# Performance work log

Hardware: AMD Instinct MI355X
Metric: run time of the kernel (lower is better)

## Reference

```python
import jax, jax.numpy as jnp
import numpy as np

BOX_SIDE = 50.0  # orthorhombic simulation cell side length


def setup_inputs() -> dict:
    key = jax.random.key(0)
    k1, _ = jax.random.split(key)
    N = 8192
    pos = jax.random.uniform(k1, (N, 3), dtype=jnp.float32) * BOX_SIDE  # cartesian positions in box
    box = jnp.ones((3,), dtype=jnp.float32) * BOX_SIDE                   # box lengths (orthorhombic)
    return {"pos": pos, "box": box, "k": 17}


def reference(pos, box, k):
    """Periodic (minimum-image) k-NN graph: returns (edge_index [2, N*k], knn_dist [N, k])."""
    N = pos.shape[0]
    # Accumulate squared wrapped distances one spatial dim at a time to avoid an (N,N,3) intermediate.
    d2 = jnp.zeros((N, N), dtype=pos.dtype)
    for d in range(pos.shape[1]):  # fixed small loop over 3 spatial dims
        diff = pos[:, None, d] - pos[None, :, d]
        diff = diff - box[d] * jnp.round(diff / box[d])  # minimum-image wrap
        d2 = d2 + diff * diff
    # Exclude self-edges.
    d2 = jnp.where(jnp.eye(N, dtype=bool), jnp.inf, d2)
    # k nearest neighbors per node (smallest distance => top_k of negated d2).
    _, idx = jax.lax.top_k(-d2, k)                      # idx: [N, k]
    knn_d2 = jnp.take_along_axis(d2, idx, axis=1)       # [N, k]
    knn_dist = jnp.sqrt(knn_d2)
    src = jnp.repeat(jnp.arange(N), k)
    edge_index = jnp.stack([src, idx.reshape(-1)])      # [2, N*k] (source, neighbor)
    return edge_index, knn_dist
```

## Files before the change

### kernel.cpp

```cpp
#include <hip/hip_runtime.h>
#include <math.h>

#define K 17
#define WAVE 64
#define G 10
#define CELLS (G*G*G)
#define BCAP 16
#define OVCAP 128
#define CAP 128
#define KEY_MAX 0xFFFFFFFFFFFFFFFFULL

__device__ __forceinline__ bool lex_less(float ad, int ai, float bd, int bi) {
    return (ad < bd) || (ad == bd && ai < bi);
}


__global__ __launch_bounds__(256) void prep_bucket(
    const float* __restrict__ pos, const float* __restrict__ box,
    int* __restrict__ cnt, int* __restrict__ ovCnt,
    float4* __restrict__ ov, float4* __restrict__ bucket, int N)
{
    const int t = blockIdx.x * 256 + threadIdx.x;
    if (t >= N) return;
    const float x = pos[3*t+0], y = pos[3*t+1], z = pos[3*t+2];
    const float invx = (float)G / box[0];
    const float invy = (float)G / box[1];
    const float invz = (float)G / box[2];
    const int cx = min((int)(x * invx), G-1);
    const int cy = min((int)(y * invy), G-1);
    const int cz = min((int)(z * invz), G-1);
    const int cell = (cz*G + cy)*G + cx;
    const int slot = atomicAdd(&cnt[cell], 1);
    const float4 v = make_float4(x, y, z, __int_as_float(t));
    if (slot < BCAP) bucket[cell*BCAP + slot] = v;
    else {
        int o = atomicAdd(ovCnt, 1);
        if (o < OVCAP) ov[o] = v;
    }
}


__global__ __launch_bounds__(256, 4) void knn_main(
    const float* __restrict__ pos, const float* __restrict__ box,
    const int* __restrict__ cnt, const int* __restrict__ ovCnt,
    const float4* __restrict__ ov, const float4* __restrict__ bucket,
    float* __restrict__ out, int N)
{
    const int lane = threadIdx.x & 63;
    const int wid  = threadIdx.x >> 6;
    const int i = blockIdx.x * 4 + wid;
    if (i >= N) return;

    __shared__ unsigned long long surv[4][CAP];

    const float bx = box[0], by = box[1], bz = box[2];
    const float hx = 0.5f*bx, hy = 0.5f*by, hz = 0.5f*bz;
    const float invx = (float)G/bx, invy = (float)G/by, invz = (float)G/bz;
    const float cmin = fminf(bx, fminf(by, bz)) / (float)G;

    const float xi = pos[3*i+0], yi = pos[3*i+1], zi = pos[3*i+2];
    const int cx = min((int)(xi*invx), G-1);
    const int cy = min((int)(yi*invy), G-1);
    const int cz = min((int)(zi*invz), G-1);

    const long kN = (long)N * K;
    const int slot = lane & 15;
    const int gq   = lane >> 4;

    int  M = 0;
    bool have = false;

    {
        const int oc = ovCnt[0];
        float4 pv[7]; int cv[7]; bool gv[7];
#pragma unroll
        for (int p = 0; p < 7; ++p) {
            const int g = 4*p + gq;
            gv[p] = (g < 27);
            int cell = 0;
            if (gv[p]) {
                int ox = g % 3 - 1, oy = (g/3) % 3 - 1, oz = g/9 - 1;
                int ux = cx + ox; ux += (ux < 0) ? G : 0; ux -= (ux >= G) ? G : 0;
                int uy = cy + oy; uy += (uy < 0) ? G : 0; uy -= (uy >= G) ? G : 0;
                int uz = cz + oz; uz += (uz < 0) ? G : 0; uz -= (uz >= G) ? G : 0;
                cell = (uz*G + uy)*G + ux;
            }
            cv[p] = cnt[cell];
            pv[p] = bucket[cell*BCAP + slot];
        }
        float4 ov0 = ov[lane];
        float4 ov1 = ov[WAVE + lane];

        const float thr = cmin * cmin * 0.999f;
        const unsigned long long thrKey =
            ((unsigned long long)__float_as_uint(thr) << 13) | 0x1FFFULL;

        int base = 0; bool bad = (oc > OVCAP);
#pragma unroll
        for (int p = 0; p < 9; ++p) {
            unsigned long long key = KEY_MAX;
            float4 pnt; bool valid;
            if (p < 7) { pnt = pv[p]; valid = gv[p] && (slot < min(cv[p], BCAP)); }
            else if (p == 7) { pnt = ov0; valid = (lane < oc); }
            else       { pnt = ov1; valid = (WAVE + lane < oc); }
            const int j = __float_as_int(pnt.w);
            if (valid && j != i) {
                float dx = __fsub_rn(xi, pnt.x);
                float dy = __fsub_rn(yi, pnt.y);
                float dz = __fsub_rn(zi, pnt.z);
                dx = dx > hx ? __fsub_rn(dx, bx) : (dx < -hx ? __fadd_rn(dx, bx) : dx);
                dy = dy > hy ? __fsub_rn(dy, by) : (dy < -hy ? __fadd_rn(dy, by) : dy);
                dz = dz > hz ? __fsub_rn(dz, bz) : (dz < -hz ? __fadd_rn(dz, bz) : dz);
                float cd = __fadd_rn(__fadd_rn(__fmul_rn(dx, dx), __fmul_rn(dy, dy)),
                                     __fmul_rn(dz, dz));
                key = ((unsigned long long)__float_as_uint(cd) << 13) | (unsigned)j;
            }
            const bool sv = (key <= thrKey);
            unsigned long long mk = __ballot(sv);
            int pc = __popcll(mk);
            if (base + pc <= CAP) {
                if (sv) {
                    int below = __popcll(mk & ((1ULL << lane) - 1ULL));
                    surv[wid][base + below] = key;
                }
            } else bad = true;
            base += pc;
        }
        if (!bad && base >= K) { have = true; M = base; }
    }

    if (!have && ovCnt[0] <= OVCAP) {
        const int oc = ovCnt[0];
        const float thr2 = cmin * cmin * 1.9580f;
        const unsigned long long thrKey2 =
            ((unsigned long long)__float_as_uint(thr2) << 13) | 0x1FFFULL;

        int base = 0; bool bad2 = false;
#pragma unroll 1
        for (int p = 0; p < 32; ++p) {
            const int g = 4*p + gq;
            unsigned long long key = KEY_MAX;
            if (g < 125) {
                int ox = g % 5 - 2, oy = (g/5) % 5 - 2, oz = g/25 - 2;
                int ux = cx + ox; ux += (ux < 0) ? G : 0; ux -= (ux >= G) ? G : 0;
                int uy = cy + oy; uy += (uy < 0) ? G : 0; uy -= (uy >= G) ? G : 0;
                int uz = cz + oz; uz += (uz < 0) ? G : 0; uz -= (uz >= G) ? G : 0;
                const int cell = (uz*G + uy)*G + ux;
                const int c = cnt[cell];
                const float4 pnt = bucket[cell*BCAP + slot];
                const int j = __float_as_int(pnt.w);
                if (slot < min(c, BCAP) && j != i) {
                    float dx = __fsub_rn(xi, pnt.x);
                    float dy = __fsub_rn(yi, pnt.y);
                    float dz = __fsub_rn(zi, pnt.z);
                    dx = dx > hx ? __fsub_rn(dx, bx) : (dx < -hx ? __fadd_rn(dx, bx) : dx);
                    dy = dy > hy ? __fsub_rn(dy, by) : (dy < -hy ? __fadd_rn(dy, by) : dy);
                    dz = dz > hz ? __fsub_rn(dz, bz) : (dz < -hz ? __fadd_rn(dz, bz) : dz);
                    float cd = __fadd_rn(__fadd_rn(__fmul_rn(dx, dx), __fmul_rn(dy, dy)),
                                         __fmul_rn(dz, dz));
                    key = ((unsigned long long)__float_as_uint(cd) << 13) | (unsigned)j;
                }
            }
            const bool sv = (key <= thrKey2);
            unsigned long long mk = __ballot(sv);
            int pc = __popcll(mk);
            if (base + pc <= CAP) {
                if (sv) {
                    int below = __popcll(mk & ((1ULL << lane) - 1ULL));
                    surv[wid][base + below] = key;
                }
            } else bad2 = true;
            base += pc;
        }
        if (!bad2 && oc > 0) {
#pragma unroll
            for (int rdx = 0; rdx < 2; ++rdx) {
                const int t = rdx*WAVE + lane;
                unsigned long long key = KEY_MAX;
                const float4 pnt = ov[t];
                const int j = __float_as_int(pnt.w);
                if (t < oc && j != i) {
                    float dx = __fsub_rn(xi, pnt.x);
                    float dy = __fsub_rn(yi, pnt.y);
                    float dz = __fsub_rn(zi, pnt.z);
                    dx = dx > hx ? __fsub_rn(dx, bx) : (dx < -hx ? __fadd_rn(dx, bx) : dx);
                    dy = dy > hy ? __fsub_rn(dy, by) : (dy < -hy ? __fadd_rn(dy, by) : dy);
                    dz = dz > hz ? __fsub_rn(dz, bz) : (dz < -hz ? __fadd_rn(dz, bz) : dz);
                    float cd = __fadd_rn(__fadd_rn(__fmul_rn(dx, dx), __fmul_rn(dy, dy)),
                                         __fmul_rn(dz, dz));
                    key = ((unsigned long long)__float_as_uint(cd) << 13) | (unsigned)j;
                }
                const bool sv = (key <= thrKey2);
                unsigned long long mk = __ballot(sv);
                int pc = __popcll(mk);
                if (base + pc <= CAP) {
                    if (sv) {
                        int below = __popcll(mk & ((1ULL << lane) - 1ULL));
                        surv[wid][base + below] = key;
                    }
                } else bad2 = true;
                base += pc;
            }
        }
        if (!bad2 && base >= K) { have = true; M = base; }
    }

    if (have) {
        __asm__ __volatile__("s_waitcnt lgkmcnt(0)" ::: "memory");
        unsigned long long k0 = surv[wid][(lane < M) ? lane : 0];
        unsigned long long k1 = (lane + 64 < M) ? surv[wid][lane + 64] : KEY_MAX;
        int r0 = 0, r1 = 0;
#pragma unroll 2
        for (int m = 0; m < M; ++m) {
            unsigned long long s = surv[wid][m];
            r0 += (s < k0) ? 1 : 0;
            r1 += (s < k1) ? 1 : 0;
        }
        if (lane < K) out[(long)i*K + lane] = (float)i;
        if (lane < M && r0 < K) {
            out[kN + (long)i*K + r0]   = (float)(int)(k0 & 0x1FFFULL);
            out[2*kN + (long)i*K + r0] = __fsqrt_rn(__uint_as_float((unsigned)(k0 >> 13)));
        }
        if (lane + 64 < M && r1 < K) {
            out[kN + (long)i*K + r1]   = (float)(int)(k1 & 0x1FFFULL);
            out[2*kN + (long)i*K + r1] = __fsqrt_rn(__uint_as_float((unsigned)(k1 >> 13)));
        }
        return;
    }

    {
        float d[K]; int id[K];
#pragma unroll
        for (int m = 0; m < K; ++m) { d[m] = INFINITY; id[m] = 0x7fffffff; }

#pragma unroll 1
        for (int j0 = 0; j0 < N; j0 += WAVE) {
            const int j = j0 + lane;
            float cd = INFINITY; int ci = 0x7fffffff;
            if (j < N && j != i) {
                float dx = __fsub_rn(xi, pos[3*j+0]);
                float dy = __fsub_rn(yi, pos[3*j+1]);
                float dz = __fsub_rn(zi, pos[3*j+2]);
                dx = dx > hx ? __fsub_rn(dx, bx) : (dx < -hx ? __fadd_rn(dx, bx) : dx);
                dy = dy > hy ? __fsub_rn(dy, by) : (dy < -hy ? __fadd_rn(dy, by) : dy);
                dz = dz > hz ? __fsub_rn(dz, bz) : (dz < -hz ? __fadd_rn(dz, bz) : dz);
                cd = __fadd_rn(__fadd_rn(__fmul_rn(dx, dx), __fmul_rn(dy, dy)),
                               __fmul_rn(dz, dz));
                ci = j;
            }
            if (lex_less(cd, ci, d[K-1], id[K-1])) {
                bool lt[K];
#pragma unroll
                for (int m = 0; m < K; ++m) lt[m] = lex_less(cd, ci, d[m], id[m]);
#pragma unroll
                for (int m = K-1; m >= 1; --m) {
                    d[m]  = lt[m-1] ? d[m-1]  : (lt[m] ? cd : d[m]);
                    id[m] = lt[m-1] ? id[m-1] : (lt[m] ? ci : id[m]);
                }
                d[0]  = lt[0] ? cd : d[0];
                id[0] = lt[0] ? ci : id[0];
            }
        }

#pragma unroll 1
        for (int e = 0; e < K; ++e) {
            float bv = d[0]; int bi = id[0];
#pragma unroll
            for (int off = 32; off >= 1; off >>= 1) {
                float ov2 = __shfl_xor(bv, off, WAVE);
                int   oi = __shfl_xor(bi, off, WAVE);
                if (lex_less(ov2, oi, bv, bi)) { bv = ov2; bi = oi; }
            }
            if (d[0] == bv && id[0] == bi) {
#pragma unroll
                for (int m = 0; m < K-1; ++m) { d[m] = d[m+1]; id[m] = id[m+1]; }
                d[K-1] = INFINITY; id[K-1] = 0x7fffffff;
            }
            if (lane == e) {
                out[kN + (long)i*K + e]   = (float)bi;
                out[2*kN + (long)i*K + e] = __fsqrt_rn(bv);
            }
        }
        if (lane < K) out[(long)i*K + lane] = (float)i;
    }
}

extern "C" void kernel_launch(void* const* d_in, const int* in_sizes, int n_in,
                              void* d_out, int out_size, void* d_ws, size_t ws_size,
                              hipStream_t stream) {
    const float* pos = (const float*)d_in[0];
    const float* box = (const float*)d_in[1];
    const int N = in_sizes[0] / 3;

    unsigned char* ws = (unsigned char*)d_ws;
    int*    cnt    = (int*)ws;
    int*    ovCnt  = (int*)(ws + 4000);
    float4* ov     = (float4*)(ws + 4096);
    float4* bucket = (float4*)(ws + 8192);

    hipMemsetAsync(cnt, 0, 4004, stream);
    prep_bucket<<<dim3((N + 255) / 256), dim3(256), 0, stream>>>(
        pos, box, cnt, ovCnt, ov, bucket, N);
    knn_main<<<dim3((N + 3) / 4), dim3(256), 0, stream>>>(
        pos, box, cnt, ovCnt, ov, bucket, (float*)d_out, N);
}
```

Measured before the change: 91.71 us.

## Precompute per-cell periodic shifts and batch fallback loads in groups of eight

Replaces the per-candidate minimum-image compare-and-select with a per-cell periodic offset worked out once from the cell wrap, so each distance needs only a subtract and an add. The 5x5x5 fallback loop now issues eight cell loads at a time before computing, hiding memory latency, and the overflow rounds are skipped when the overflow list is empty. Shared ballot and compaction code is moved into lambdas. Because the offset is tied to the cell wrap rather than to the actual displacement, results could differ from the reference rounding in edge cases, and the batched loads raise register pressure.

```diff
diff --git a/kernel.cpp b/kernel.cpp
--- a/kernel.cpp
+++ b/kernel.cpp
@@ -70,61 +70,95 @@
     int  M = 0;
     bool have = false;
 
+    int  base = 0;
+    bool bad  = false;
+
+    auto flush = [&](unsigned long long key, unsigned long long tk) {
+        const bool sv = (key <= tk);
+        unsigned long long mk = __ballot(sv);
+        int pc = __popcll(mk);
+        if (base + pc <= CAP) {
+            if (sv) {
+                int below = __popcll(mk & ((1ULL << lane) - 1ULL));
+                surv[wid][base + below] = key;
+            }
+        } else bad = true;
+        base += pc;
+    };
+
+    auto round_mi = [&](float4 pnt, bool valid, unsigned long long tk) {
+        unsigned long long key = KEY_MAX;
+        const int j = __float_as_int(pnt.w);
+        if (valid && j != i) {
+            float dx = __fsub_rn(xi, pnt.x);
+            float dy = __fsub_rn(yi, pnt.y);
+            float dz = __fsub_rn(zi, pnt.z);
+            dx = dx > hx ? __fsub_rn(dx, bx) : (dx < -hx ? __fadd_rn(dx, bx) : dx);
+            dy = dy > hy ? __fsub_rn(dy, by) : (dy < -hy ? __fadd_rn(dy, by) : dy);
+            dz = dz > hz ? __fsub_rn(dz, bz) : (dz < -hz ? __fadd_rn(dz, bz) : dz);
+            float cd = __fadd_rn(__fadd_rn(__fmul_rn(dx, dx), __fmul_rn(dy, dy)),
+                                 __fmul_rn(dz, dz));
+            key = ((unsigned long long)__float_as_uint(cd) << 13) | (unsigned)j;
+        }
+        flush(key, tk);
+    };
+
     {
         const int oc = ovCnt[0];
         float4 pv[7]; int cv[7]; bool gv[7];
+        float wox[7], woy[7], woz[7];
 #pragma unroll
         for (int p = 0; p < 7; ++p) {
             const int g = 4*p + gq;
             gv[p] = (g < 27);
-            int cell = 0;
+            int cell = 0; float wx = 0.f, wy = 0.f, wz = 0.f;
             if (gv[p]) {
                 int ox = g % 3 - 1, oy = (g/3) % 3 - 1, oz = g/9 - 1;
-                int ux = cx + ox; ux += (ux < 0) ? G : 0; ux -= (ux >= G) ? G : 0;
-                int uy = cy + oy; uy += (uy < 0) ? G : 0; uy -= (uy >= G) ? G : 0;
-                int uz = cz + oz; uz += (uz < 0) ? G : 0; uz -= (uz >= G) ? G : 0;
+                int ux = cx + ox;
+                if (ux < 0)       { ux += G; wx =  bx; }
+                else if (ux >= G) { ux -= G; wx = -bx; }
+                int uy = cy + oy;
+                if (uy < 0)       { uy += G; wy =  by; }
+                else if (uy >= G) { uy -= G; wy = -by; }
+                int uz = cz + oz;
+                if (uz < 0)       { uz += G; wz =  bz; }
+                else if (uz >= G) { uz -= G; wz = -bz; }
                 cell = (uz*G + uy)*G + ux;
             }
             cv[p] = cnt[cell];
             pv[p] = bucket[cell*BCAP + slot];
+            wox[p] = wx; woy[p] = wy; woz[p] = wz;
         }
         float4 ov0 = ov[lane];
         float4 ov1 = ov[WAVE + lane];
+
+        bool vm[7];
+#pragma unroll
+        for (int p = 0; p < 7; ++p) vm[p] = gv[p] && (slot < min(cv[p], BCAP));
 
         const float thr = cmin * cmin * 0.999f;
         const unsigned long long thrKey =
             ((unsigned long long)__float_as_uint(thr) << 13) | 0x1FFFULL;
 
-        int base = 0; bool bad = (oc > OVCAP);
-#pragma unroll
-        for (int p = 0; p < 9; ++p) {
+        base = 0; bad = (oc > OVCAP);
+#pragma unroll
+        for (int p = 0; p < 7; ++p) {
             unsigned long long key = KEY_MAX;
-            float4 pnt; bool valid;
-            if (p < 7) { pnt = pv[p]; valid = gv[p] && (slot < min(cv[p], BCAP)); }
-            else if (p == 7) { pnt = ov0; valid = (lane < oc); }
-            else       { pnt = ov1; valid = (WAVE + lane < oc); }
+            const float4 pnt = pv[p];
             const int j = __float_as_int(pnt.w);
-            if (valid && j != i) {
-                float dx = __fsub_rn(xi, pnt.x);
-                float dy = __fsub_rn(yi, pnt.y);
-                float dz = __fsub_rn(zi, pnt.z);
-                dx = dx > hx ? __fsub_rn(dx, bx) : (dx < -hx ? __fadd_rn(dx, bx) : dx);
-                dy = dy > hy ? __fsub_rn(dy, by) : (dy < -hy ? __fadd_rn(dy, by) : dy);
-                dz = dz > hz ? __fsub_rn(dz, bz) : (dz < -hz ? __fadd_rn(dz, bz) : dz);
+            if (vm[p] && j != i) {
+                float dx = __fadd_rn(__fsub_rn(xi, pnt.x), wox[p]);
+                float dy = __fadd_rn(__fsub_rn(yi, pnt.y), woy[p]);
+                float dz = __fadd_rn(__fsub_rn(zi, pnt.z), woz[p]);
                 float cd = __fadd_rn(__fadd_rn(__fmul_rn(dx, dx), __fmul_rn(dy, dy)),
                                      __fmul_rn(dz, dz));
                 key = ((unsigned long long)__float_as_uint(cd) << 13) | (unsigned)j;
             }
-            const bool sv = (key <= thrKey);
-            unsigned long long mk = __ballot(sv);
-            int pc = __popcll(mk);
-            if (base + pc <= CAP) {
-                if (sv) {
-                    int below = __popcll(mk & ((1ULL << lane) - 1ULL));
-                    surv[wid][base + below] = key;
-                }
-            } else bad = true;
-            base += pc;
+            flush(key, thrKey);
+        }
+        if (oc > 0) {
+            round_mi(ov0, lane < oc, thrKey);
+            round_mi(ov1, WAVE + lane < oc, thrKey);
         }
         if (!bad && base >= K) { have = true; M = base; }
     }
@@ -135,74 +169,54 @@
         const unsigned long long thrKey2 =
             ((unsigned long long)__float_as_uint(thr2) << 13) | 0x1FFFULL;
 
-        int base = 0; bool bad2 = false;
+        base = 0; bad = false;
 #pragma unroll 1
-        for (int p = 0; p < 32; ++p) {
-            const int g = 4*p + gq;
-            unsigned long long key = KEY_MAX;
-            if (g < 125) {
-                int ox = g % 5 - 2, oy = (g/5) % 5 - 2, oz = g/25 - 2;
-                int ux = cx + ox; ux += (ux < 0) ? G : 0; ux -= (ux >= G) ? G : 0;
-                int uy = cy + oy; uy += (uy < 0) ? G : 0; uy -= (uy >= G) ? G : 0;
-                int uz = cz + oz; uz += (uz < 0) ? G : 0; uz -= (uz >= G) ? G : 0;
-                const int cell = (uz*G + uy)*G + ux;
-                const int c = cnt[cell];
-                const float4 pnt = bucket[cell*BCAP + slot];
+        for (int b = 0; b < 4; ++b) {
+            float4 pv2[8]; int cv2[8]; bool gv2[8];
+            float wx2[8], wy2[8], wz2[8];
+#pragma unroll
+            for (int q = 0; q < 8; ++q) {
+                const int g = 4*(8*b + q) + gq;
+                gv2[q] = (g < 125);
+                int cell = 0; float wx = 0.f, wy = 0.f, wz = 0.f;
+                if (gv2[q]) {
+                    int ox = g % 5 - 2, oy = (g/5) % 5 - 2, oz = g/25 - 2;
+                    int ux = cx + ox;
+                    if (ux < 0)       { ux += G; wx =  bx; }
+                    else if (ux >= G) { ux -= G; wx = -bx; }
+                    int uy = cy + oy;
+                    if (uy < 0)       { uy += G; wy =  by; }
+                    else if (uy >= G) { uy -= G; wy = -by; }
+                    int uz = cz + oz;
+                    if (uz < 0)       { uz += G; wz =  bz; }
+                    else if (uz >= G) { uz -= G; wz = -bz; }
+                    cell = (uz*G + uy)*G + ux;
+                }
+                cv2[q] = cnt[cell];
+                pv2[q] = bucket[cell*BCAP + slot];
+                wx2[q] = wx; wy2[q] = wy; wz2[q] = wz;
+            }
+#pragma unroll
+            for (int q = 0; q < 8; ++q) {
+                unsigned long long key = KEY_MAX;
+                const float4 pnt = pv2[q];
                 const int j = __float_as_int(pnt.w);
-                if (slot < min(c, BCAP) && j != i) {
-                    float dx = __fsub_rn(xi, pnt.x);
-                    float dy = __fsub_rn(yi, pnt.y);
-                    float dz = __fsub_rn(zi, pnt.z);
-                    dx = dx > hx ? __fsub_rn(dx, bx) : (dx < -hx ? __fadd_rn(dx, bx) : dx);
-                    dy = dy > hy ? __fsub_rn(dy, by) : (dy < -hy ? __fadd_rn(dy, by) : dy);
-                    dz = dz > hz ? __fsub_rn(dz, bz) : (dz < -hz ? __fadd_rn(dz, bz) : dz);
+                if (gv2[q] && (slot < min(cv2[q], BCAP)) && j != i) {
+                    float dx = __fadd_rn(__fsub_rn(xi, pnt.x), wx2[q]);
+                    float dy = __fadd_rn(__fsub_rn(yi, pnt.y), wy2[q]);
+                    float dz = __fadd_rn(__fsub_rn(zi, pnt.z), wz2[q]);
                     float cd = __fadd_rn(__fadd_rn(__fmul_rn(dx, dx), __fmul_rn(dy, dy)),
                                          __fmul_rn(dz, dz));
                     key = ((unsigned long long)__float_as_uint(cd) << 13) | (unsigned)j;
                 }
-            }
-            const bool sv = (key <= thrKey2);
-            unsigned long long mk = __ballot(sv);
-            int pc = __popcll(mk);
-            if (base + pc <= CAP) {
-                if (sv) {
-                    int below = __popcll(mk & ((1ULL << lane) - 1ULL));
-                    surv[wid][base + below] = key;
-                }
-            } else bad2 = true;
-            base += pc;
-        }
-        if (!bad2 && oc > 0) {
-#pragma unroll
-            for (int rdx = 0; rdx < 2; ++rdx) {
-                const int t = rdx*WAVE + lane;
-                unsigned long long key = KEY_MAX;
-                const float4 pnt = ov[t];
-                const int j = __float_as_int(pnt.w);
-                if (t < oc && j != i) {
-                    float dx = __fsub_rn(xi, pnt.x);
-                    float dy = __fsub_rn(yi, pnt.y);
-                    float dz = __fsub_rn(zi, pnt.z);
-                    dx = dx > hx ? __fsub_rn(dx, bx) : (dx < -hx ? __fadd_rn(dx, bx) : dx);
-                    dy = dy > hy ? __fsub_rn(dy, by) : (dy < -hy ? __fadd_rn(dy, by) : dy);
-                    dz = dz > hz ? __fsub_rn(dz, bz) : (dz < -hz ? __fadd_rn(dz, bz) : dz);
-                    float cd = __fadd_rn(__fadd_rn(__fmul_rn(dx, dx), __fmul_rn(dy, dy)),
-                                         __fmul_rn(dz, dz));
-                    key = ((unsigned long long)__float_as_uint(cd) << 13) | (unsigned)j;
-                }
-                const bool sv = (key <= thrKey2);
-                unsigned long long mk = __ballot(sv);
-                int pc = __popcll(mk);
-                if (base + pc <= CAP) {
-                    if (sv) {
-                        int below = __popcll(mk & ((1ULL << lane) - 1ULL));
-                        surv[wid][base + below] = key;
-                    }
-                } else bad2 = true;
-                base += pc;
-            }
-        }
-        if (!bad2 && base >= K) { have = true; M = base; }
+                flush(key, thrKey2);
+            }
+        }
+        if (!bad && oc > 0) {
+            round_mi(ov[lane],        lane < oc,        thrKey2);
+            round_mi(ov[WAVE + lane], WAVE + lane < oc, thrKey2);
+        }
+        if (!bad && base >= K) { have = true; M = base; }
     }
 
     if (have) {
```

Result: faster. 85.56 us (-6.7%).
